# Performance work log

Hardware: AMD Instinct MI355X
Metric: run time of the kernel (lower is better)

Reference implementation:

```python
import jax, jax.numpy as jnp
import numpy as np
from itertools import combinations

B, F, K, V = 1024, 39, 16, 200000  # batch, fields, embed dim, vocab
EPS = 1e-3  # tf.layers.batch_normalization default epsilon


def setup_inputs() -> dict:
    key = jax.random.key(0)
    ks = jax.random.split(key, 6)
    pairs = np.array(list(combinations(range(F), 2)), dtype=np.int32)   # [741, 2]
    trips = np.array(list(combinations(range(F), 3)), dtype=np.int32)   # [9139, 3]
    P, T = pairs.shape[0], trips.shape[0]
    return {
        "feats": jax.random.randint(ks[0], (B, F), 0, V, dtype=jnp.int32),
        "w": jax.random.normal(ks[1], (V,), dtype=jnp.float32) * 0.01,
        "v": jax.random.normal(ks[2], (V, K), dtype=jnp.float32) * 0.01,
        "b": jnp.zeros((1,), dtype=jnp.float32),
        "gamma2": jnp.ones((P,), dtype=jnp.float32),
        "beta2": jnp.zeros((P,), dtype=jnp.float32),
        "gw2": jax.random.uniform(ks[3], (P,), minval=0.599, maxval=0.601, dtype=jnp.float32),
        "gamma3": jnp.ones((T,), dtype=jnp.float32),
        "beta3": jnp.zeros((T,), dtype=jnp.float32),
        "gw3": jax.random.uniform(ks[4], (T,), minval=0.599, maxval=0.601, dtype=jnp.float32),
        "rows": jnp.asarray(pairs[:, 1]),   # second element of each pair
        "cols": jnp.asarray(pairs[:, 0]),   # first element of each pair
        "i1": jnp.asarray(trips[:, 0]),
        "i2": jnp.asarray(trips[:, 1]),
        "i3": jnp.asarray(trips[:, 2]),
    }


def _batchnorm(x, gamma, beta):
    # training-mode BN over batch axis; x: [B, P]
    m = jnp.mean(x, axis=0)
    var = jnp.mean(jnp.square(x - m), axis=0)
    return (x - m) * jax.lax.rsqrt(var + EPS) * gamma + beta


def reference(feats, w, v, b, gamma2, beta2, gw2, gamma3, beta3, gw3,
              rows, cols, i1, i2, i3):
    xw = w[feats]            # [B, F]  first-order weights
    xv = v[feats]            # [B, F, K] embeddings
    l = jnp.sum(xw, axis=1)  # linear term [B]

    # second-order: gather pair embeddings, multiply, reduce over K
    level2 = jnp.sum(xv[:, rows, :] * xv[:, cols, :], axis=-1)  # [B, P]
    level2 = _batchnorm(level2, gamma2, beta2) * gw2            # soft mask
    fm_out = jnp.sum(level2, axis=-1)                           # [B]

    # third-order: gather triple embeddings
    level3 = jnp.sum(xv[:, i1, :] * xv[:, i2, :] * xv[:, i3, :], axis=-1)  # [B, T]
    level3 = _batchnorm(level3, gamma3, beta3) * gw3
    fm_out2 = jnp.sum(level3, axis=-1)                          # [B]

    logits = l + fm_out + fm_out2 + b[0]                        # [B]
    return logits
```

## Files before the change

### kernel.cpp

```cpp
#include <hip/hip_runtime.h>
#include <math.h>

#define B_ 1024
#define F_ 39
#define K_ 16
#define P_ 741
#define T_ 9139
#define NC_ 9880
#define EPS_ 1e-3f
#define ESTR 18
#define LS2 9920

__device__ __forceinline__ unsigned short to_bf16(float x) {
    unsigned u = __float_as_uint(x);
    u += 0x7fffu + ((u >> 16) & 1u);
    return (unsigned short)(u >> 16);
}
__device__ __forceinline__ float from_bf16(unsigned short h) {
    return __uint_as_float(((unsigned)h) << 16);
}

__global__ __launch_bounds__(256) void pack_k(const int* __restrict__ rows,
                                              const int* __restrict__ cols,
                                              const int* __restrict__ i1,
                                              const int* __restrict__ i2,
                                              const int* __restrict__ i3,
                                              unsigned* __restrict__ pidx) {
    int c = blockIdx.x * 256 + threadIdx.x;
    if (c >= NC_) return;
    unsigned pk;
    if (c < P_) {
        pk = (unsigned)(cols[c] * ESTR) | ((unsigned)(rows[c] * ESTR) << 10);
    } else {
        int t = c - P_;
        int a = i1[t], b = i2[t], cc = i3[t];
        int p = a * (2 * F_ - 1 - a) / 2 + (b - a - 1);
        pk = (unsigned)p | ((unsigned)(cc * ESTR) << 10);
    }
    pidx[c] = pk;
}

__global__ __launch_bounds__(256) void levels_k(const int* __restrict__ feats,
                                                const float* __restrict__ v,
                                                const unsigned* __restrict__ pidx,
                                                unsigned short* __restrict__ levels) {
    int b = blockIdx.x;
    int tid = threadIdx.x;
    __shared__ int   tok[F_];
    __shared__ float emb[F_ * ESTR];
    __shared__ float Y[P_ * K_];
    __shared__ unsigned short buf[LS2];

    if (tid < F_) tok[tid] = feats[b * F_ + tid];
    __syncthreads();
    for (int idx = tid; idx < F_ * K_; idx += 256) {
        int f = idx >> 4, k = idx & 15;
        emb[f * ESTR + k] = v[(size_t)tok[f] * K_ + k];
    }
    __syncthreads();

    for (int p = tid; p < P_; p += 256) {
        unsigned pk = pidx[p];
        int o1 = (int)(pk & 1023u);
        int o2 = (int)((pk >> 10) & 1023u);
        float s = 0.f;
#pragma unroll
        for (int j = 0; j < 8; ++j) {
            float2 a = *(const float2*)&emb[o1 + 2 * j];
            float2 c = *(const float2*)&emb[o2 + 2 * j];
            float2 y = make_float2(a.x * c.x, a.y * c.y);
            *(float2*)&Y[p * K_ + 2 * j] = y;
            s += y.x + y.y;
        }
        buf[p] = to_bf16(s);
    }
    __syncthreads();

#pragma unroll 1
    for (int i = 0; i < (T_ + 255) / 256; ++i) {
        int t = i * 256 + tid;
        if (t < T_) {
            unsigned pk = pidx[P_ + t];
            int p  = (int)(pk & 1023u);
            int o3 = (int)((pk >> 10) & 1023u);
            float s = 0.f;
#pragma unroll
            for (int j = 0; j < 8; ++j) {
                float2 y = *(const float2*)&Y[p * K_ + 2 * j];
                float2 e = *(const float2*)&emb[o3 + 2 * j];
                s += y.x * e.x + y.y * e.y;
            }
            buf[P_ + t] = to_bf16(s);
        }
    }
    if (tid < LS2 - NC_) buf[NC_ + tid] = 0;
    __syncthreads();

    uint4* dst = (uint4*)(levels + (size_t)b * LS2);
    const uint4* src = (const uint4*)buf;
    for (int idx = tid; idx < LS2 / 8; idx += 256)
        dst[idx] = src[idx];
}

__global__ __launch_bounds__(256) void stats2_k(const unsigned short* __restrict__ levels,
                                                float* __restrict__ colsum,
                                                float* __restrict__ colsumsq) {
    int col = blockIdx.x * 256 + threadIdx.x;
    if (col >= NC_) return;
    const unsigned short* p = levels + (size_t)(blockIdx.y * 16) * LS2 + col;
    float s1 = 0.f, s2 = 0.f;
#pragma unroll
    for (int r = 0; r < 16; ++r) {
        float x = from_bf16(p[(size_t)r * LS2]);
        s1 += x;
        s2 += x * x;
    }
    atomicAdd(&colsum[col], s1);
    atomicAdd(&colsumsq[col], s2);
}

__global__ __launch_bounds__(256) void finalize_k(const float* __restrict__ colsum,
                                                  const float* __restrict__ colsumsq,
                                                  const float* __restrict__ gamma2,
                                                  const float* __restrict__ beta2,
                                                  const float* __restrict__ gw2,
                                                  const float* __restrict__ gamma3,
                                                  const float* __restrict__ beta3,
                                                  const float* __restrict__ gw3,
                                                  float* __restrict__ scale,
                                                  float* __restrict__ Cacc) {
    int col = blockIdx.x * 256 + threadIdx.x;
    float c = 0.f;
    if (col < NC_) {
        float mean = colsum[col] * (1.0f / B_);
        float var  = colsumsq[col] * (1.0f / B_) - mean * mean;
        float inv  = 1.0f / sqrtf(var + EPS_);
        float g, be, gw;
        if (col < P_) {
            g = gamma2[col]; be = beta2[col]; gw = gw2[col];
        } else {
            int t = col - P_;
            g = gamma3[t]; be = beta3[t]; gw = gw3[t];
        }
        scale[col] = gw * g * inv;
        c = gw * (be - g * inv * mean);
    }
    __shared__ float red[256];
    red[threadIdx.x] = c;
    __syncthreads();
    for (int s = 128; s > 0; s >>= 1) {
        if (threadIdx.x < s) red[threadIdx.x] += red[threadIdx.x + s];
        __syncthreads();
    }
    if (threadIdx.x == 0) atomicAdd(Cacc, red[0]);
}

__global__ __launch_bounds__(256) void out_k(const unsigned short* __restrict__ levels,
                                             const float* __restrict__ scale,
                                             const int* __restrict__ feats,
                                             const float* __restrict__ w,
                                             const float* __restrict__ Cacc,
                                             const float* __restrict__ bias,
                                             float* __restrict__ out) {
    int b = blockIdx.x, tid = threadIdx.x;
    const uint2* lv = (const uint2*)(levels + (size_t)b * LS2);
    float acc = 0.f;
    for (int idx = tid; idx < 2470; idx += 256) {
        uint2 u = lv[idx];
        int cbase = idx * 4;
        float4 sc = *(const float4*)&scale[cbase];
        float x0 = __uint_as_float(u.x << 16);
        float x1 = __uint_as_float(u.x & 0xffff0000u);
        float x2 = __uint_as_float(u.y << 16);
        float x3 = __uint_as_float(u.y & 0xffff0000u);
        acc += sc.x * x0 + sc.y * x1 + sc.z * x2 + sc.w * x3;
    }
    if (tid < F_) acc += w[feats[b * F_ + tid]];
    __shared__ float red[256];
    red[tid] = acc;
    __syncthreads();
    for (int s = 128; s > 0; s >>= 1) {
        if (tid < s) red[tid] += red[tid + s];
        __syncthreads();
    }
    if (tid == 0) out[b] = red[0] + Cacc[0] + bias[0];
}

extern "C" void kernel_launch(void* const* d_in, const int* in_sizes, int n_in,
                              void* d_out, int out_size, void* d_ws, size_t ws_size,
                              hipStream_t stream) {
    const int*   feats  = (const int*)d_in[0];
    const float* w      = (const float*)d_in[1];
    const float* v      = (const float*)d_in[2];
    const float* bias   = (const float*)d_in[3];
    const float* gamma2 = (const float*)d_in[4];
    const float* beta2  = (const float*)d_in[5];
    const float* gw2    = (const float*)d_in[6];
    const float* gamma3 = (const float*)d_in[7];
    const float* beta3  = (const float*)d_in[8];
    const float* gw3    = (const float*)d_in[9];
    const int*   rows   = (const int*)d_in[10];
    const int*   cols   = (const int*)d_in[11];
    const int*   i1     = (const int*)d_in[12];
    const int*   i2     = (const int*)d_in[13];
    const int*   i3     = (const int*)d_in[14];
    float*       out    = (float*)d_out;
    float*       ws     = (float*)d_ws;

    float*          scale    = ws;
    float*          colsum   = ws + 9880;
    float*          colsumsq = ws + 19760;
    float*          Cacc     = ws + 29640;
    unsigned*       pidx     = (unsigned*)(ws + 29696);
    unsigned short* levels   = (unsigned short*)(ws + 39680);

    hipMemsetAsync(colsum, 0, (size_t)(2 * NC_ + 1) * sizeof(float), stream);

    pack_k<<<(NC_ + 255) / 256, 256, 0, stream>>>(rows, cols, i1, i2, i3, pidx);
    levels_k<<<B_, 256, 0, stream>>>(feats, v, pidx, levels);
    stats2_k<<<dim3((NC_ + 255) / 256, B_ / 16), 256, 0, stream>>>(levels, colsum, colsumsq);
    finalize_k<<<(NC_ + 255) / 256, 256, 0, stream>>>(colsum, colsumsq,
                                                      gamma2, beta2, gw2,
                                                      gamma3, beta3, gw3, scale, Cacc);
    out_k<<<B_, 256, 0, stream>>>(levels, scale, feats, w, Cacc, bias, out);
}
```

Before: 152.5 us.

## Store embeddings and pair products as bf16 in LDS, 512-thread blocks per two rows

The levels kernel now keeps the embeddings and pairwise products in shared memory as bf16 with a stride of 20 instead of fp32. This shrinks LDS use and halves the shared-memory read traffic in the triple loop. It also runs 512-thread blocks that each handle two batch rows in sequence. The hipMemsetAsync is folded into the index-packing kernel, which removes one launch. In exchange, the intermediate pair products are rounded to bf16 before the third-order reduction, which adds numerical error.

New measurement: 159.0 us. 4.3% more time.

```diff
diff --git a/kernel.cpp b/kernel.cpp
--- a/kernel.cpp
+++ b/kernel.cpp
@@ -8,7 +8,7 @@
 #define T_ 9139
 #define NC_ 9880
 #define EPS_ 1e-3f
-#define ESTR 18
+#define S2 20
 #define LS2 9920
 
 __device__ __forceinline__ unsigned short to_bf16(float x) {
@@ -19,87 +19,110 @@
 __device__ __forceinline__ float from_bf16(unsigned short h) {
     return __uint_as_float(((unsigned)h) << 16);
 }
-
-__global__ __launch_bounds__(256) void pack_k(const int* __restrict__ rows,
+__device__ __forceinline__ float2 bf2x(unsigned u) {
+    return make_float2(__uint_as_float(u << 16), __uint_as_float(u & 0xffff0000u));
+}
+
+__global__ __launch_bounds__(256) void prep_k(const int* __restrict__ rows,
                                               const int* __restrict__ cols,
                                               const int* __restrict__ i1,
                                               const int* __restrict__ i2,
                                               const int* __restrict__ i3,
-                                              unsigned* __restrict__ pidx) {
+                                              unsigned* __restrict__ pidx,
+                                              float* __restrict__ colsum,
+                                              float* __restrict__ colsumsq,
+                                              float* __restrict__ Cacc) {
     int c = blockIdx.x * 256 + threadIdx.x;
     if (c >= NC_) return;
+    colsum[c] = 0.f;
+    colsumsq[c] = 0.f;
+    if (c == 0) Cacc[0] = 0.f;
     unsigned pk;
     if (c < P_) {
-        pk = (unsigned)(cols[c] * ESTR) | ((unsigned)(rows[c] * ESTR) << 10);
+        pk = (unsigned)(cols[c] * S2) | ((unsigned)(rows[c] * S2) << 10);
     } else {
         int t = c - P_;
         int a = i1[t], b = i2[t], cc = i3[t];
         int p = a * (2 * F_ - 1 - a) / 2 + (b - a - 1);
-        pk = (unsigned)p | ((unsigned)(cc * ESTR) << 10);
+        pk = (unsigned)p | ((unsigned)(cc * S2) << 10);
     }
     pidx[c] = pk;
 }
 
-__global__ __launch_bounds__(256) void levels_k(const int* __restrict__ feats,
+__global__ __launch_bounds__(512) void levels_k(const int* __restrict__ feats,
                                                 const float* __restrict__ v,
                                                 const unsigned* __restrict__ pidx,
                                                 unsigned short* __restrict__ levels) {
-    int b = blockIdx.x;
     int tid = threadIdx.x;
-    __shared__ int   tok[F_];
-    __shared__ float emb[F_ * ESTR];
-    __shared__ float Y[P_ * K_];
-    __shared__ unsigned short buf[LS2];
-
-    if (tid < F_) tok[tid] = feats[b * F_ + tid];
-    __syncthreads();
-    for (int idx = tid; idx < F_ * K_; idx += 256) {
-        int f = idx >> 4, k = idx & 15;
-        emb[f * ESTR + k] = v[(size_t)tok[f] * K_ + k];
-    }
-    __syncthreads();
-
-    for (int p = tid; p < P_; p += 256) {
-        unsigned pk = pidx[p];
-        int o1 = (int)(pk & 1023u);
-        int o2 = (int)((pk >> 10) & 1023u);
-        float s = 0.f;
-#pragma unroll
-        for (int j = 0; j < 8; ++j) {
-            float2 a = *(const float2*)&emb[o1 + 2 * j];
-            float2 c = *(const float2*)&emb[o2 + 2 * j];
-            float2 y = make_float2(a.x * c.x, a.y * c.y);
-            *(float2*)&Y[p * K_ + 2 * j] = y;
-            s += y.x + y.y;
-        }
-        buf[p] = to_bf16(s);
-    }
-    __syncthreads();
+    __shared__ int tok[F_];
+    __shared__ __attribute__((aligned(16))) unsigned short emb2[F_ * S2];
+    __shared__ __attribute__((aligned(16))) unsigned short Y2[P_ * S2];
+    __shared__ __attribute__((aligned(16))) unsigned short buf[LS2];
 
 #pragma unroll 1
-    for (int i = 0; i < (T_ + 255) / 256; ++i) {
-        int t = i * 256 + tid;
-        if (t < T_) {
-            unsigned pk = pidx[P_ + t];
-            int p  = (int)(pk & 1023u);
-            int o3 = (int)((pk >> 10) & 1023u);
+    for (int rr = 0; rr < 2; ++rr) {
+        int b = 2 * blockIdx.x + rr;
+        __syncthreads();
+        if (tid < F_) tok[tid] = feats[b * F_ + tid];
+        __syncthreads();
+        for (int idx = tid; idx < F_ * K_; idx += 512) {
+            int f = idx >> 4, k = idx & 15;
+            emb2[f * S2 + k] = to_bf16(v[(size_t)tok[f] * K_ + k]);
+        }
+        __syncthreads();
+
+#pragma unroll 1
+        for (int p = tid; p < P_; p += 512) {
+            unsigned pk = pidx[p];
+            int o1 = (int)(pk & 1023u);
+            int o2 = (int)((pk >> 10) & 1023u);
             float s = 0.f;
 #pragma unroll
-            for (int j = 0; j < 8; ++j) {
-                float2 y = *(const float2*)&Y[p * K_ + 2 * j];
-                float2 e = *(const float2*)&emb[o3 + 2 * j];
-                s += y.x * e.x + y.y * e.y;
+            for (int j = 0; j < 4; ++j) {
+                uint2 ua = *(const uint2*)&emb2[o1 + 4 * j];
+                uint2 uc = *(const uint2*)&emb2[o2 + 4 * j];
+                float2 a0 = bf2x(ua.x), a1 = bf2x(ua.y);
+                float2 c0 = bf2x(uc.x), c1 = bf2x(uc.y);
+                float y0 = a0.x * c0.x, y1 = a0.y * c0.y;
+                float y2 = a1.x * c1.x, y3 = a1.y * c1.y;
+                s += y0 + y1 + y2 + y3;
+                uint2 pk2;
+                pk2.x = (unsigned)to_bf16(y0) | ((unsigned)to_bf16(y1) << 16);
+                pk2.y = (unsigned)to_bf16(y2) | ((unsigned)to_bf16(y3) << 16);
+                *(uint2*)&Y2[p * S2 + 4 * j] = pk2;
             }
-            buf[P_ + t] = to_bf16(s);
-        }
-    }
-    if (tid < LS2 - NC_) buf[NC_ + tid] = 0;
-    __syncthreads();
-
-    uint4* dst = (uint4*)(levels + (size_t)b * LS2);
-    const uint4* src = (const uint4*)buf;
-    for (int idx = tid; idx < LS2 / 8; idx += 256)
-        dst[idx] = src[idx];
+            buf[p] = to_bf16(s);
+        }
+        __syncthreads();
+
+#pragma unroll 1
+        for (int i = 0; i < (T_ + 511) / 512; ++i) {
+            int t = i * 512 + tid;
+            if (t < T_) {
+                unsigned pk = pidx[P_ + t];
+                int p  = (int)(pk & 1023u);
+                int o3 = (int)((pk >> 10) & 1023u);
+                int yb = p * S2;
+                float s = 0.f;
+#pragma unroll
+                for (int j = 0; j < 4; ++j) {
+                    uint2 uy = *(const uint2*)&Y2[yb + 4 * j];
+                    uint2 ue = *(const uint2*)&emb2[o3 + 4 * j];
+                    float2 y0 = bf2x(uy.x), y1 = bf2x(uy.y);
+                    float2 e0 = bf2x(ue.x), e1 = bf2x(ue.y);
+                    s += y0.x * e0.x + y0.y * e0.y + y1.x * e1.x + y1.y * e1.y;
+                }
+                buf[P_ + t] = to_bf16(s);
+            }
+        }
+        if (tid < LS2 - NC_) buf[NC_ + tid] = 0;
+        __syncthreads();
+
+        uint4* dst = (uint4*)(levels + (size_t)b * LS2);
+        const uint4* src = (const uint4*)buf;
+        for (int idx = tid; idx < LS2 / 8; idx += 512)
+            dst[idx] = src[idx];
+    }
 }
 
 __global__ __launch_bounds__(256) void stats2_k(const unsigned short* __restrict__ levels,
@@ -214,10 +237,9 @@
     unsigned*       pidx     = (unsigned*)(ws + 29696);
     unsigned short* levels   = (unsigned short*)(ws + 39680);
 
-    hipMemsetAsync(colsum, 0, (size_t)(2 * NC_ + 1) * sizeof(float), stream);
-
-    pack_k<<<(NC_ + 255) / 256, 256, 0, stream>>>(rows, cols, i1, i2, i3, pidx);
-    levels_k<<<B_, 256, 0, stream>>>(feats, v, pidx, levels);
+    prep_k<<<(NC_ + 255) / 256, 256, 0, stream>>>(rows, cols, i1, i2, i3,
+                                                  pidx, colsum, colsumsq, Cacc);
+    levels_k<<<B_ / 2, 512, 0, stream>>>(feats, v, pidx, levels);
     stats2_k<<<dim3((NC_ + 255) / 256, B_ / 16), 256, 0, stream>>>(levels, colsum, colsumsq);
     finalize_k<<<(NC_ + 255) / 256, 256, 0, stream>>>(colsum, colsumsq,
                                                       gamma2, beta2, gw2,
```
